# Kernel optimization log

Hardware: AMD Instinct MI355X
Metric: run time of the kernel (lower is better)

The kernel has to match this reference:

```python
import jax, jax.numpy as jnp
import numpy as np

NUM_STAGES = 2
DE_NEIGHBORS = 3

def _square_distance(a, b):
    # a: [B,N,3], b: [B,S,3] -> [B,N,S] squared euclidean distances
    return (jnp.sum(a * a, axis=-1)[:, :, None]
            + jnp.sum(b * b, axis=-1)[:, None, :]
            - 2.0 * jnp.einsum('bnc,bsc->bns', a, b))

def _propagate(xyz1, xyz2, points1, points2, k):
    # xyz1:[B,N,3] fine, xyz2:[B,S,3] coarse, points1:[B,D1,N], points2:[B,D2,S]
    p2 = jnp.transpose(points2, (0, 2, 1))  # [B,S,D2]
    B, N, _ = xyz1.shape
    S = xyz2.shape[1]
    if S == 1:
        interp = jnp.broadcast_to(p2, (B, N, p2.shape[-1]))
    else:
        d = _square_distance(xyz1, xyz2)              # [B,N,S]
        neg_top, idx = jax.lax.top_k(-d, k)           # k smallest distances
        dists = -neg_top                              # [B,N,k]
        recip = 1.0 / (dists + 1e-8)
        weight = recip / jnp.sum(recip, axis=2, keepdims=True)  # [B,N,k]
        # gather neighbor features: [B,N,k,D2]
        gathered = jnp.take_along_axis(p2[:, None, :, :], idx[..., None], axis=2)
        interp = jnp.sum(gathered * weight[..., None], axis=2)  # [B,N,D2]
    if points1 is not None:
        p1 = jnp.transpose(points1, (0, 2, 1))        # [B,N,D1]
        new = jnp.concatenate([p1, interp], axis=-1)
    else:
        new = interp
    return jnp.transpose(new, (0, 2, 1))              # [B,D1+D2,N]

def setup_inputs() -> dict:
    key = jax.random.key(0)
    ks = jax.random.split(key, 6)
    return {
        'xyz0': jax.random.normal(ks[0], (4, 8192, 3), dtype=jnp.float32),
        'xyz1': jax.random.normal(ks[1], (4, 2048, 3), dtype=jnp.float32),
        'xyz2': jax.random.normal(ks[2], (4, 512, 3), dtype=jnp.float32),
        'x0': jax.random.normal(ks[3], (4, 128, 8192), dtype=jnp.float32),
        'x1': jax.random.normal(ks[4], (4, 256, 2048), dtype=jnp.float32),
        'x2': jax.random.normal(ks[5], (4, 512, 512), dtype=jnp.float32),
    }

def reference(xyz0, xyz1, xyz2, x0, x1, x2):
    # original forward reverses the lists; emulate with pre-reversed lists
    xyz_list = [xyz2, xyz1, xyz0]   # coarse -> fine
    x_list = [x2, x1, x0]
    x = x_list[0]
    for i in range(NUM_STAGES):
        x = _propagate(xyz_list[i + 1], xyz_list[i], x_list[i + 1], x, DE_NEIGHBORS)
    return x  # [4, 896, 8192]
```

## Files before the change

kernel.cpp:

```cpp
#include <hip/hip_runtime.h>

#define BIG 3.0e38f

typedef float vf4 __attribute__((ext_vector_type(4)));

__device__ __forceinline__ vf4 ld4(const float* p) { return *(const vf4*)p; }

__device__ __forceinline__ void insert3(float d, int s,
                                        float& d0, float& d1, float& d2,
                                        int& i0, int& i1, int& i2) {
    const bool b0 = d < d0;
    const bool b1 = d < d1;
    const bool b2 = d < d2;
    i2 = b1 ? i1 : (b2 ? s : i2);
    i1 = b0 ? i0 : (b1 ? s : i1);
    i0 = b0 ? s  : i0;
    const float nd1 = __builtin_amdgcn_fmed3f(d, d0, d1);
    d2 = __builtin_amdgcn_fmed3f(d, d1, d2);
    d0 = fminf(d, d0);
    d1 = nd1;
}

__device__ __forceinline__ void insert3_tie(float d, int s,
                                            float& d0, float& d1, float& d2,
                                            int& i0, int& i1, int& i2) {
    const bool b0 = (d < d0) | ((d == d0) & (s < i0));
    const bool b1 = (d < d1) | ((d == d1) & (s < i1));
    const bool b2 = (d < d2) | ((d == d2) & (s < i2));
    i2 = b1 ? i1 : (b2 ? s : i2);
    i1 = b0 ? i0 : (b1 ? s : i1);
    i0 = b0 ? s  : i0;
    d2 = b1 ? d1 : (b2 ? d : d2);
    d1 = b0 ? d0 : (b1 ? d : d1);
    d0 = b0 ? d  : d0;
}

template <int S, int PHASES>
__device__ void knn_tile(const float* __restrict__ xyzF, const float* __restrict__ xyzC,
                         int N, int b, int nb,
                         int* __restrict__ idx, float* __restrict__ w,
                         void* smem) {
    constexpr int H   = S / PHASES;
    constexpr int SPC = H / 8;
    float4* sc  = (float4*)smem;
    float*  smd = (float*)((char*)smem + H * 16);
    int*    smi = (int*)((char*)smem + H * 16 + 3072);
    const int tid = threadIdx.x;
    const int q   = tid & 31;
    const int sp  = tid >> 5;
    const int n   = nb + q;
    const float ax = xyzF[(b * N + n) * 3 + 0];
    const float ay = xyzF[(b * N + n) * 3 + 1];
    const float az = xyzF[(b * N + n) * 3 + 2];

    float d0 = BIG, d1 = BIG, d2 = BIG;
    int i0 = 0, i1 = 0, i2 = 0;

    for (int ph = 0; ph < PHASES; ++ph) {
        const int base = ph * H;
        if (ph) __syncthreads();
        for (int i = tid; i < H; i += 256) {
            const float x = xyzC[(b * S + base + i) * 3 + 0];
            const float y = xyzC[(b * S + base + i) * 3 + 1];
            const float z = xyzC[(b * S + base + i) * 3 + 2];
            sc[i] = make_float4(x, y, z, 0.5f * (x * x + y * y + z * z));
        }
        __syncthreads();
        const int s0 = sp * SPC;
#pragma unroll 8
        for (int t = 0; t < SPC; ++t) {
            const float4 p = sc[s0 + t];
            const float h = fmaf(-ax, p.x, fmaf(-ay, p.y, fmaf(-az, p.z, p.w)));
            insert3(h, base + s0 + t, d0, d1, d2, i0, i1, i2);
        }
    }

    smd[tid * 3 + 0] = d0; smi[tid * 3 + 0] = i0;
    smd[tid * 3 + 1] = d1; smi[tid * 3 + 1] = i1;
    smd[tid * 3 + 2] = d2; smi[tid * 3 + 2] = i2;
    __syncthreads();

    if (tid < 32) {
        float e0 = BIG, e1 = BIG, e2 = BIG;
        int j0 = 0, j1 = 0, j2 = 0;
#pragma unroll
        for (int ch = 0; ch < 8; ++ch) {
#pragma unroll
            for (int k = 0; k < 3; ++k) {
                insert3_tie(smd[(ch * 32 + tid) * 3 + k], smi[(ch * 32 + tid) * 3 + k],
                            e0, e1, e2, j0, j1, j2);
            }
        }
        const float an = ax * ax + ay * ay + az * az;
        const float r0 = 1.0f / (fmaf(2.0f, e0, an) + 1e-8f);
        const float r1 = 1.0f / (fmaf(2.0f, e1, an) + 1e-8f);
        const float r2 = 1.0f / (fmaf(2.0f, e2, an) + 1e-8f);
        const float rs = r0 + r1 + r2;
        const int nn = nb + tid;
        idx[(b * 3 + 0) * N + nn] = j0;
        idx[(b * 3 + 1) * N + nn] = j1;
        idx[(b * 3 + 2) * N + nn] = j2;
        w[(b * 3 + 0) * N + nn] = r0 / rs;
        w[(b * 3 + 1) * N + nn] = r1 / rs;
        w[(b * 3 + 2) * N + nn] = r2 / rs;
    }
}

__device__ void transpose_tile(const float* __restrict__ in, float* __restrict__ out,
                               int C, int N, int OS,
                               int b, int nb, int cb, void* smem) {
    float (*s)[65] = (float (*)[65])smem;
    const int lo = threadIdx.x & 63;
    const int r  = threadIdx.x >> 6;
#pragma unroll
    for (int i = 0; i < 16; ++i) {
        const int cl = r + 4 * i;
        s[cl][lo] = in[((size_t)b * C + cb + cl) * N + nb + lo];
    }
    __syncthreads();
#pragma unroll
    for (int i = 0; i < 16; ++i) {
        const int pl = r + 4 * i;
        out[((size_t)b * N + nb + pl) * OS + cb + lo] = s[lo][pl];
    }
}

__global__ __launch_bounds__(256) void k1_stage(const float* __restrict__ xyz0,
                                                const float* __restrict__ xyz1,
                                                const float* __restrict__ xyz2,
                                                const float* __restrict__ x1,
                                                const float* __restrict__ x2,
                                                float* __restrict__ x1P,
                                                float* __restrict__ x2P,
                                                int* __restrict__ idx1,
                                                float* __restrict__ w1,
                                                int* __restrict__ idx2,
                                                float* __restrict__ w2) {
    __shared__ float4 smem4[1408];
    const int id = blockIdx.x;
    if (id < 1024) {
        const int b  = id >> 8;
        const int nb = (id & 255) * 32;
        knn_tile<2048, 2>(xyz0, xyz1, 8192, b, nb, idx2, w2, smem4);
    } else if (id < 1280) {
        const int r  = id - 1024;
        const int b  = r >> 6;
        const int nb = (r & 63) * 32;
        knn_tile<512, 1>(xyz1, xyz2, 2048, b, nb, idx1, w1, smem4);
    } else if (id < 1536) {
        const int r  = id - 1280;
        const int b  = r >> 6;
        const int nb = (r & 7) * 64;
        const int cb = ((r >> 3) & 7) * 64;
        transpose_tile(x2, x2P, 512, 512, 512, b, nb, cb, smem4);
    } else {
        const int r  = id - 1536;
        const int b  = r >> 7;
        const int nb = (r & 31) * 64;
        const int cb = ((r >> 5) & 3) * 64;
        transpose_tile(x1, x1P, 256, 2048, 256, b, nb, cb, smem4);
    }
}

__global__ __launch_bounds__(256) void k2_final(const float* __restrict__ x0,
                                                const float* __restrict__ x1P,
                                                const float* __restrict__ x2P,
                                                const int* __restrict__ idx1,
                                                const float* __restrict__ w1,
                                                const int* __restrict__ idx2,
                                                const float* __restrict__ w2,
                                                float* __restrict__ out) {
    __shared__ vf4 smemv[1376];
    float (*tile)[68] = (float (*)[68])smemv;
    int*   sj9 = (int*)((float*)smemv + 4352);
    float* sw9 = (float*)((float*)smemv + 4928);
    const int id  = blockIdx.x;
    const int tid = threadIdx.x;
    const int q4  = tid & 15;
    const int pg  = (tid >> 4) & 3;
    const int r   = tid >> 6;

    if (id < 1024) {
        const int b     = id >> 8;
        const int rem   = id & 255;
        const int ntile = rem >> 1;
        const int cq    = rem & 1;
        const int nb    = ntile * 64;

        if (tid < 192) {
            const int p = tid & 63, k = tid >> 6;
            const int   j  = idx2[(b * 3 + k) * 8192 + nb + p];
            const float wk = w2[(b * 3 + k) * 8192 + nb + p];
#pragma unroll
            for (int m = 0; m < 3; ++m) {
                sj9[(k * 3 + m) * 64 + p] = idx1[(b * 3 + m) * 2048 + j] * 512;
                sw9[(k * 3 + m) * 64 + p] = wk * w1[(b * 3 + m) * 2048 + j];
            }
        }
        __syncthreads();

        for (int ct = 0; ct < 4; ++ct) {
            const int cb = (cq * 4 + ct) * 64;
            const float* xb = x2P + (size_t)b * 512 * 512 + cb + q4 * 4;
#pragma unroll
            for (int i = 0; i < 4; ++i) {
                const int p = i * 16 + r * 4 + pg;
                vf4 acc = sw9[0 * 64 + p] * ld4(xb + sj9[0 * 64 + p]);
#pragma unroll
                for (int j = 1; j < 9; ++j) {
                    acc += sw9[j * 64 + p] * ld4(xb + sj9[j * 64 + p]);
                }
                *(vf4*)&tile[p][q4 * 4] = acc;
            }
            __syncthreads();
            {
                const int p2 = tid & 63;
#pragma unroll
                for (int i = 0; i < 16; ++i) {
                    const int cl = r + 4 * i;
                    __builtin_nontemporal_store(tile[p2][cl],
                        &out[((size_t)b * 896 + 384 + cb + cl) * 8192 + nb + p2]);
                }
            }
            __syncthreads();
        }
    } else if (id < 3072) {
        const int t     = id - 1024;
        const int b     = t >> 9;
        const int rem   = t & 511;
        const int ntile = rem >> 2;
        const int ct    = rem & 3;
        const int nb    = ntile * 64;
        const int cb    = ct * 64;
        int*   sj1 = sj9;
        float* sw1 = sw9;

        if (tid < 192) {
            const int p = tid & 63, k = tid >> 6;
            sj1[k * 64 + p] = idx2[(b * 3 + k) * 8192 + nb + p] * 256;
            sw1[k * 64 + p] = w2[(b * 3 + k) * 8192 + nb + p];
        }
        __syncthreads();

        const float* xb = x1P + (size_t)b * 2048 * 256 + cb + q4 * 4;
#pragma unroll
        for (int i = 0; i < 4; ++i) {
            const int p = i * 16 + r * 4 + pg;
            const vf4 acc = sw1[0 * 64 + p] * ld4(xb + sj1[0 * 64 + p])
                          + sw1[1 * 64 + p] * ld4(xb + sj1[1 * 64 + p])
                          + sw1[2 * 64 + p] * ld4(xb + sj1[2 * 64 + p]);
            *(vf4*)&tile[p][q4 * 4] = acc;
        }
        __syncthreads();
        {
            const int p2 = tid & 63;
#pragma unroll
            for (int i = 0; i < 16; ++i) {
                const int cl = r + 4 * i;
                __builtin_nontemporal_store(tile[p2][cl],
                    &out[((size_t)b * 896 + 128 + cb + cl) * 8192 + nb + p2]);
            }
        }
    } else {
        const int rr = id - 3072;
        const int b  = rr >> 6;
        const int lb = rr & 63;
        const vf4* src = (const vf4*)x0;
        vf4* dst = (vf4*)out;
#pragma unroll
        for (int t2 = 0; t2 < 16; ++t2) {
            const int i = lb * 4096 + t2 * 256 + tid;
            const vf4 v = __builtin_nontemporal_load(&src[(size_t)b * (128 * 2048) + i]);
            __builtin_nontemporal_store(v, &dst[(size_t)b * (896 * 2048) + i]);
        }
    }
}

extern "C" void kernel_launch(void* const* d_in, const int* in_sizes, int n_in,
                              void* d_out, int out_size, void* d_ws, size_t ws_size,
                              hipStream_t stream) {
    const float* xyz0 = (const float*)d_in[0];
    const float* xyz1 = (const float*)d_in[1];
    const float* xyz2 = (const float*)d_in[2];
    const float* x0   = (const float*)d_in[3];
    const float* x1   = (const float*)d_in[4];
    const float* x2   = (const float*)d_in[5];
    float* out = (float*)d_out;

    char* ws = (char*)d_ws;
    float* x1P  = (float*)(ws + 0);
    float* x2P  = (float*)(ws + 8388608);
    int*   idx1 = (int*)(ws + 12582912);
    float* w1   = (float*)(ws + 12681216);
    int*   idx2 = (int*)(ws + 12779520);
    float* w2   = (float*)(ws + 13172736);

    k1_stage<<<dim3(2048), 256, 0, stream>>>(xyz0, xyz1, xyz2, x1, x2,
                                             x1P, x2P, idx1, w1, idx2, w2);
    k2_final<<<dim3(3328), 256, 0, stream>>>(x0, x1P, x2P, idx1, w1, idx2, w2, out);
}
```

Before: 204.4 us.

## Materialize stage-1 interpolated features instead of composing 9-neighbor weights

Instead of composing both interpolation stages into a 9-tap gather from x2 per fine point, a new kernel first computes the stage-1 interpolated features (2048 points x 512 channels, point-major) into workspace. The final kernel then does a 3-tap gather from that buffer, with more, smaller blocks. Nontemporal loads and stores are also replaced by regular ones. The cost is an extra kernel launch and a 16 MB intermediate write and read, in exchange for fewer gather loads per output element.

```diff
diff --git a/kernel.cpp b/kernel.cpp
--- a/kernel.cpp
+++ b/kernel.cpp
@@ -162,83 +162,101 @@
     }
 }
 
-__global__ __launch_bounds__(256) void k2_final(const float* __restrict__ x0,
+__global__ __launch_bounds__(256) void interp1_pm(const float* __restrict__ x2P,
+                                                  const int* __restrict__ idx1,
+                                                  const float* __restrict__ w1,
+                                                  float* __restrict__ featP2) {
+    __shared__ int   sj[3 * 64];
+    __shared__ float sw[3 * 64];
+    const int id = blockIdx.x;
+    const int b  = id >> 8;
+    const int nt = (id >> 3) & 31;
+    const int ct = id & 7;
+    const int nb = nt * 64;
+    const int cb = ct * 64;
+    const int tid = threadIdx.x;
+
+    if (tid < 192) {
+        const int p = tid & 63, k = tid >> 6;
+        sj[k * 64 + p] = idx1[(b * 3 + k) * 2048 + nb + p] * 512;
+        sw[k * 64 + p] = w1[(b * 3 + k) * 2048 + nb + p];
+    }
+    __syncthreads();
+
+    const int q4 = tid & 15, pg = (tid >> 4) & 3, r = tid >> 6;
+    const float* xb = x2P + (size_t)b * 512 * 512 + cb + q4 * 4;
+    float* fb = featP2 + ((size_t)b * 2048 + nb) * 512 + cb + q4 * 4;
+#pragma unroll
+    for (int i = 0; i < 4; ++i) {
+        const int p = i * 16 + r * 4 + pg;
+        const vf4 acc = sw[0 * 64 + p] * ld4(xb + sj[0 * 64 + p])
+                      + sw[1 * 64 + p] * ld4(xb + sj[1 * 64 + p])
+                      + sw[2 * 64 + p] * ld4(xb + sj[2 * 64 + p]);
+        *(vf4*)(fb + (size_t)p * 512) = acc;
+    }
+}
+
+__global__ __launch_bounds__(256) void k3_final(const float* __restrict__ x0,
                                                 const float* __restrict__ x1P,
-                                                const float* __restrict__ x2P,
-                                                const int* __restrict__ idx1,
-                                                const float* __restrict__ w1,
+                                                const float* __restrict__ featP2,
                                                 const int* __restrict__ idx2,
                                                 const float* __restrict__ w2,
                                                 float* __restrict__ out) {
-    __shared__ vf4 smemv[1376];
-    float (*tile)[68] = (float (*)[68])smemv;
-    int*   sj9 = (int*)((float*)smemv + 4352);
-    float* sw9 = (float*)((float*)smemv + 4928);
+    __shared__ float tile[64][68];
+    __shared__ int   sj[3 * 64];
+    __shared__ float sw[3 * 64];
     const int id  = blockIdx.x;
     const int tid = threadIdx.x;
     const int q4  = tid & 15;
     const int pg  = (tid >> 4) & 3;
     const int r   = tid >> 6;
 
-    if (id < 1024) {
-        const int b     = id >> 8;
-        const int rem   = id & 255;
-        const int ntile = rem >> 1;
-        const int cq    = rem & 1;
-        const int nb    = ntile * 64;
+    if (id < 4096) {
+        const int b   = id >> 10;
+        const int rem = id & 1023;
+        const int nt  = rem >> 3;
+        const int ct  = rem & 7;
+        const int nb  = nt * 64;
+        const int cb  = ct * 64;
 
         if (tid < 192) {
             const int p = tid & 63, k = tid >> 6;
-            const int   j  = idx2[(b * 3 + k) * 8192 + nb + p];
-            const float wk = w2[(b * 3 + k) * 8192 + nb + p];
-#pragma unroll
-            for (int m = 0; m < 3; ++m) {
-                sj9[(k * 3 + m) * 64 + p] = idx1[(b * 3 + m) * 2048 + j] * 512;
-                sw9[(k * 3 + m) * 64 + p] = wk * w1[(b * 3 + m) * 2048 + j];
+            sj[k * 64 + p] = idx2[(b * 3 + k) * 8192 + nb + p] * 512;
+            sw[k * 64 + p] = w2[(b * 3 + k) * 8192 + nb + p];
+        }
+        __syncthreads();
+
+        const float* xb = featP2 + (size_t)b * 2048 * 512 + cb + q4 * 4;
+#pragma unroll
+        for (int i = 0; i < 4; ++i) {
+            const int p = i * 16 + r * 4 + pg;
+            const vf4 acc = sw[0 * 64 + p] * ld4(xb + sj[0 * 64 + p])
+                          + sw[1 * 64 + p] * ld4(xb + sj[1 * 64 + p])
+                          + sw[2 * 64 + p] * ld4(xb + sj[2 * 64 + p]);
+            *(vf4*)&tile[p][q4 * 4] = acc;
+        }
+        __syncthreads();
+        {
+            const int p2 = tid & 63;
+#pragma unroll
+            for (int i = 0; i < 16; ++i) {
+                const int cl = r + 4 * i;
+                out[((size_t)b * 896 + 384 + cb + cl) * 8192 + nb + p2] = tile[p2][cl];
             }
         }
-        __syncthreads();
-
-        for (int ct = 0; ct < 4; ++ct) {
-            const int cb = (cq * 4 + ct) * 64;
-            const float* xb = x2P + (size_t)b * 512 * 512 + cb + q4 * 4;
-#pragma unroll
-            for (int i = 0; i < 4; ++i) {
-                const int p = i * 16 + r * 4 + pg;
-                vf4 acc = sw9[0 * 64 + p] * ld4(xb + sj9[0 * 64 + p]);
-#pragma unroll
-                for (int j = 1; j < 9; ++j) {
-                    acc += sw9[j * 64 + p] * ld4(xb + sj9[j * 64 + p]);
-                }
-                *(vf4*)&tile[p][q4 * 4] = acc;
-            }
-            __syncthreads();
-            {
-                const int p2 = tid & 63;
-#pragma unroll
-                for (int i = 0; i < 16; ++i) {
-                    const int cl = r + 4 * i;
-                    __builtin_nontemporal_store(tile[p2][cl],
-                        &out[((size_t)b * 896 + 384 + cb + cl) * 8192 + nb + p2]);
-                }
-            }
-            __syncthreads();
-        }
-    } else if (id < 3072) {
-        const int t     = id - 1024;
-        const int b     = t >> 9;
-        const int rem   = t & 511;
-        const int ntile = rem >> 2;
-        const int ct    = rem & 3;
-        const int nb    = ntile * 64;
-        const int cb    = ct * 64;
-        int*   sj1 = sj9;
-        float* sw1 = sw9;
+    } else if (id < 6144) {
+        const int t   = id - 4096;
+        const int b   = t >> 9;
+        const int rem = t & 511;
+        const int nt  = rem >> 2;
+        const int ct  = rem & 3;
+        const int nb  = nt * 64;
+        const int cb  = ct * 64;
 
         if (tid < 192) {
             const int p = tid & 63, k = tid >> 6;
-            sj1[k * 64 + p] = idx2[(b * 3 + k) * 8192 + nb + p] * 256;
-            sw1[k * 64 + p] = w2[(b * 3 + k) * 8192 + nb + p];
+            sj[k * 64 + p] = idx2[(b * 3 + k) * 8192 + nb + p] * 256;
+            sw[k * 64 + p] = w2[(b * 3 + k) * 8192 + nb + p];
         }
         __syncthreads();
 
@@ -246,9 +264,9 @@
 #pragma unroll
         for (int i = 0; i < 4; ++i) {
             const int p = i * 16 + r * 4 + pg;
-            const vf4 acc = sw1[0 * 64 + p] * ld4(xb + sj1[0 * 64 + p])
-                          + sw1[1 * 64 + p] * ld4(xb + sj1[1 * 64 + p])
-                          + sw1[2 * 64 + p] * ld4(xb + sj1[2 * 64 + p]);
+            const vf4 acc = sw[0 * 64 + p] * ld4(xb + sj[0 * 64 + p])
+                          + sw[1 * 64 + p] * ld4(xb + sj[1 * 64 + p])
+                          + sw[2 * 64 + p] * ld4(xb + sj[2 * 64 + p]);
             *(vf4*)&tile[p][q4 * 4] = acc;
         }
         __syncthreads();
@@ -257,12 +275,11 @@
 #pragma unroll
             for (int i = 0; i < 16; ++i) {
                 const int cl = r + 4 * i;
-                __builtin_nontemporal_store(tile[p2][cl],
-                    &out[((size_t)b * 896 + 128 + cb + cl) * 8192 + nb + p2]);
+                out[((size_t)b * 896 + 128 + cb + cl) * 8192 + nb + p2] = tile[p2][cl];
             }
         }
     } else {
-        const int rr = id - 3072;
+        const int rr = id - 6144;
         const int b  = rr >> 6;
         const int lb = rr & 63;
         const vf4* src = (const vf4*)x0;
@@ -270,8 +287,7 @@
 #pragma unroll
         for (int t2 = 0; t2 < 16; ++t2) {
             const int i = lb * 4096 + t2 * 256 + tid;
-            const vf4 v = __builtin_nontemporal_load(&src[(size_t)b * (128 * 2048) + i]);
-            __builtin_nontemporal_store(v, &dst[(size_t)b * (896 * 2048) + i]);
+            dst[(size_t)b * (896 * 2048) + i] = src[(size_t)b * (128 * 2048) + i];
         }
     }
 }
@@ -288,14 +304,16 @@
     float* out = (float*)d_out;
 
     char* ws = (char*)d_ws;
-    float* x1P  = (float*)(ws + 0);
-    float* x2P  = (float*)(ws + 8388608);
-    int*   idx1 = (int*)(ws + 12582912);
-    float* w1   = (float*)(ws + 12681216);
-    int*   idx2 = (int*)(ws + 12779520);
-    float* w2   = (float*)(ws + 13172736);
+    float* x1P    = (float*)(ws + 0);
+    float* x2P    = (float*)(ws + 8388608);
+    float* featP2 = (float*)(ws + 12582912);
+    int*   idx1   = (int*)(ws + 29360128);
+    float* w1     = (float*)(ws + 29458432);
+    int*   idx2   = (int*)(ws + 29556736);
+    float* w2     = (float*)(ws + 29949952);
 
     k1_stage<<<dim3(2048), 256, 0, stream>>>(xyz0, xyz1, xyz2, x1, x2,
                                              x1P, x2P, idx1, w1, idx2, w2);
-    k2_final<<<dim3(3328), 256, 0, stream>>>(x0, x1P, x2P, idx1, w1, idx2, w2, out);
-}
+    interp1_pm<<<dim3(1024), 256, 0, stream>>>(x2P, idx1, w1, featP2);
+    k3_final<<<dim3(6400), 256, 0, stream>>>(x0, x1P, featP2, idx2, w2, out);
+}
```

Result: no change. 200.5 us (-1.9%).
